# Kernel optimization log

Hardware: AMD Instinct MI355X
Metric: run time of the kernel (lower is better)

Reference implementation:

```python
import jax, jax.numpy as jnp
import numpy as np

N_NODES = 50000
N_EDGES = 1600000
IN_CH = 128
HIDDEN = 64
OUT_DIM = 64
N_GRAPHS = 64


def setup_inputs() -> dict:
    key = jax.random.key(0)
    ks = jax.random.split(key, 8)
    x = jax.random.normal(ks[0], (N_NODES, IN_CH), dtype=jnp.float32)
    W1 = jax.random.normal(ks[1], (IN_CH, HIDDEN), dtype=jnp.float32) * (1.0 / np.sqrt(IN_CH))
    b1 = jnp.zeros((HIDDEN,), dtype=jnp.float32)
    W2 = jax.random.normal(ks[2], (HIDDEN, HIDDEN), dtype=jnp.float32) * (1.0 / np.sqrt(HIDDEN))
    b2 = jnp.zeros((HIDDEN,), dtype=jnp.float32)
    Wp = jax.random.normal(ks[3], (HIDDEN, OUT_DIM), dtype=jnp.float32) * (1.0 / np.sqrt(HIDDEN))
    bp = jnp.zeros((OUT_DIM,), dtype=jnp.float32)
    edge_index = jax.random.randint(ks[4], (2, N_EDGES), 0, N_NODES, dtype=jnp.int32)
    batch = jnp.sort(jax.random.randint(ks[5], (N_NODES,), 0, N_GRAPHS, dtype=jnp.int32))
    return {"x": x, "W1": W1, "b1": b1, "W2": W2, "b2": b2,
            "Wp": Wp, "bp": bp, "edge_index": edge_index, "batch": batch}


def _gcn_norm(edge_index, num_nodes):
    # add self-loops, then symmetric normalization D^{-1/2} (A+I) D^{-1/2}
    loop = jnp.arange(num_nodes, dtype=edge_index.dtype)
    src = jnp.concatenate([edge_index[0], loop])
    dst = jnp.concatenate([edge_index[1], loop])
    deg = jax.ops.segment_sum(jnp.ones_like(dst, dtype=jnp.float32), dst,
                              num_segments=num_nodes)
    dinv = jnp.where(deg > 0, jax.lax.rsqrt(deg), 0.0)
    norm = dinv[src] * dinv[dst]  # [E+N]
    return src, dst, norm


def _gcn_conv(x, W, b, src, dst, norm, num_nodes):
    h = x @ W                                  # [N, F_out] transform first (F_out small)
    msg = h[src] * norm[:, None]               # gather + scale  [E+N, F_out]
    agg = jax.ops.segment_sum(msg, dst, num_segments=num_nodes)
    return agg + b


def reference(x, W1, b1, W2, b2, Wp, bp, edge_index, batch):
    n = x.shape[0]
    src, dst, norm = _gcn_norm(edge_index, n)
    h = jax.nn.relu(_gcn_conv(x, W1, b1, src, dst, norm, n))
    # dropout: eval mode (identity)
    h = jax.nn.relu(_gcn_conv(h, W2, b2, src, dst, norm, n))
    # global mean pool over graphs in batch
    gsum = jax.ops.segment_sum(h, batch, num_segments=N_GRAPHS)
    cnt = jax.ops.segment_sum(jnp.ones((n,), dtype=h.dtype), batch,
                              num_segments=N_GRAPHS)
    g = gsum / jnp.maximum(cnt, 1.0)[:, None]
    return g @ Wp + bp
```

## Files before the change

### kernel.cpp

```cpp
#include <hip/hip_runtime.h>

#define N_NODES  50000
#define N_EDGESC 1600000
#define N_GRAPHS 64
#define NBUCK    196
#define CHUNK    2048
#define NBLK     782

static __device__ __forceinline__ unsigned short f2bf(float f) {
  unsigned u = __float_as_uint(f);
  u += 0x7FFF + ((u >> 16) & 1);
  return (unsigned short)(u >> 16);
}
static __device__ __forceinline__ float bfLo(unsigned u) {
  return __uint_as_float(u << 16);
}
static __device__ __forceinline__ float bfHi(unsigned u) {
  return __uint_as_float(u & 0xFFFF0000u);
}

static __device__ __forceinline__ int lowerb(const int* a, int n, int v) {
  int lo = 0, hi = n;
  while (lo < hi) { int m = (lo + hi) >> 1; if (a[m] < v) lo = m + 1; else hi = m; }
  return lo;
}

__global__ __launch_bounds__(256) void k_hist(const int* __restrict__ dst,
                                              int* __restrict__ bcnt,
                                              float* __restrict__ gsum, int E) {
  __shared__ int hist[NBUCK];
  int t = threadIdx.x, blk = blockIdx.x;
  if (t < NBUCK) hist[t] = 0;
  if (blk == 0) {
    for (int i = t; i < N_GRAPHS * 64; i += 256) gsum[i] = 0.f;
  }
  __syncthreads();
  int e0 = blk * CHUNK;
#pragma unroll
  for (int i = 0; i < CHUNK; i += 256) {
    int e = e0 + i + t;
    if (e < E) atomicAdd(&hist[dst[e] >> 8], 1);
  }
  __syncthreads();
  if (t < NBUCK) bcnt[(size_t)t * NBLK + blk] = hist[t];
}

__global__ __launch_bounds__(256) void k_cscan(int* __restrict__ bcnt,
                                               int* __restrict__ btot) {
  __shared__ int sm[256];
  int b = blockIdx.x, t = threadIdx.x;
  int* p = bcnt + (size_t)b * NBLK;
  int carry = 0;
  for (int tile = 0; tile < (NBLK + 255) / 256; ++tile) {
    int idx = tile * 256 + t;
    int v = (idx < NBLK) ? p[idx] : 0;
    sm[t] = v;
    __syncthreads();
    for (int o = 1; o < 256; o <<= 1) {
      int add = (t >= o) ? sm[t - o] : 0;
      __syncthreads();
      sm[t] += add;
      __syncthreads();
    }
    int incl = sm[t];
    int total = sm[255];
    if (idx < NBLK) p[idx] = incl - v + carry;
    carry += total;
    __syncthreads();
  }
  if (t == 0) btot[b] = carry;
}

__global__ __launch_bounds__(256) void k_scatter(const int* __restrict__ src,
                                                 const int* __restrict__ dst,
                                                 const int* __restrict__ bcnt,
                                                 const int* __restrict__ btot,
                                                 unsigned* __restrict__ bbuf, int E) {
  __shared__ int base[NBUCK], cur[NBUCK], sm[256];
  int t = threadIdx.x, blk = blockIdx.x;
  int v = (t < NBUCK) ? btot[t] : 0;
  sm[t] = v;
  __syncthreads();
  for (int o = 1; o < 256; o <<= 1) {
    int add = (t >= o) ? sm[t - o] : 0;
    __syncthreads();
    sm[t] += add;
    __syncthreads();
  }
  if (t < NBUCK) {
    base[t] = (sm[t] - v) + bcnt[(size_t)t * NBLK + blk];
    cur[t] = 0;
  }
  __syncthreads();
  int e0 = blk * CHUNK;
#pragma unroll
  for (int i = 0; i < CHUNK; i += 256) {
    int e = e0 + i + t;
    if (e < E) {
      int d = dst[e], b = d >> 8;
      int pos = base[b] + atomicAdd(&cur[b], 1);
      bbuf[pos] = ((unsigned)(d & 255) << 24) | (unsigned)src[e];
    }
  }
}

__global__ __launch_bounds__(512) void k_bsort(const unsigned* __restrict__ bbuf,
                                               const int* __restrict__ btot,
                                               int* __restrict__ csr,
                                               int* __restrict__ row_off,
                                               float* __restrict__ dinv) {
  __shared__ int hist[256], off[256], cur[256], sm[256];
  int b = blockIdx.x, t = threadIdx.x;
  if (t < 256) {
    int v = (t < NBUCK) ? btot[t] : 0;
    sm[t] = v;
    hist[t] = 0; cur[t] = 0;
  }
  __syncthreads();
  for (int o = 1; o < 256; o <<= 1) {
    int add = 0;
    if (t < 256 && t >= o) add = sm[t - o];
    __syncthreads();
    if (t < 256) sm[t] += add;
    __syncthreads();
  }
  int gb = (b > 0) ? sm[b - 1] : 0;
  int cnt = btot[b];
  const unsigned* bp = bbuf + gb;
  for (int i = t; i < cnt; i += 512) atomicAdd(&hist[bp[i] >> 24], 1);
  __syncthreads();
  if (t < 256) off[t] = hist[t];
  __syncthreads();
  for (int o = 1; o < 256; o <<= 1) {
    int add = 0;
    if (t < 256 && t >= o) add = off[t - o];
    __syncthreads();
    if (t < 256) off[t] += add;
    __syncthreads();
  }
  if (t < 256) {
    int excl = off[t] - hist[t];
    off[t] = excl;
    int idx = (b << 8) + t;
    if (idx <= N_NODES) row_off[idx] = gb + excl;
    if (idx < N_NODES)  dinv[idx] = rsqrtf((float)(hist[t] + 1));
  }
  __syncthreads();
  for (int i = t; i < cnt; i += 512) {
    unsigned v = bp[i];
    int ld = v >> 24;
    int pos = atomicAdd(&cur[ld], 1);
    csr[gb + off[ld] + pos] = (int)(v & 0xFFFFFFu);
  }
}

template <int K>
__global__ __launch_bounds__(256) void k_gemm(const float* __restrict__ x,
                                              const float* __restrict__ W,
                                              const float* __restrict__ dinv,
                                              unsigned short* __restrict__ out, int N) {
  constexpr int KS = 64;
  constexpr int KP = KS + 4;
  __shared__ float xs[64 * KP];
  __shared__ float Wl[KS * 64];
  const int t = threadIdx.x;
  const int lane = t & 63;
  const int w = t >> 6;
  const int n0 = blockIdx.x * 64;

  float acc[16];
#pragma unroll
  for (int j = 0; j < 16; ++j) acc[j] = 0.f;

  for (int h = 0; h < K / KS; ++h) {
#pragma unroll
    for (int i = 0; i < KS * 16 / 256; ++i) {
      int li = i * 256 + t;
      float4 v = reinterpret_cast<const float4*>(W + h * KS * 64)[li];
      *reinterpret_cast<float4*>(Wl + li * 4) = v;
    }
#pragma unroll
    for (int i = 0; i < 64 * (KS / 4) / 256; ++i) {
      int li = i * 256 + t;
      int row = li / (KS / 4), c4 = li % (KS / 4);
      int node = n0 + row;
      float4 v = make_float4(0.f, 0.f, 0.f, 0.f);
      if (node < N) v = reinterpret_cast<const float4*>(x + (size_t)node * K + h * KS)[c4];
      *reinterpret_cast<float4*>(xs + row * KP + c4 * 4) = v;
    }
    __syncthreads();

    const float* xr = xs + lane * KP;
    const float* wq = Wl + w * 16;
#pragma unroll 4
    for (int kp = 0; kp < KS / 4; ++kp) {
      float4 xv = *reinterpret_cast<const float4*>(xr + kp * 4);
#pragma unroll
      for (int q = 0; q < 4; ++q) {
        int k = kp * 4 + q;
        float xq = (q == 0) ? xv.x : (q == 1) ? xv.y : (q == 2) ? xv.z : xv.w;
        const float* wk = wq + k * 64;
        float4 w0 = *reinterpret_cast<const float4*>(wk);
        float4 w1 = *reinterpret_cast<const float4*>(wk + 4);
        float4 w2 = *reinterpret_cast<const float4*>(wk + 8);
        float4 w3 = *reinterpret_cast<const float4*>(wk + 12);
        acc[ 0] = fmaf(xq, w0.x, acc[ 0]);
        acc[ 1] = fmaf(xq, w0.y, acc[ 1]);
        acc[ 2] = fmaf(xq, w0.z, acc[ 2]);
        acc[ 3] = fmaf(xq, w0.w, acc[ 3]);
        acc[ 4] = fmaf(xq, w1.x, acc[ 4]);
        acc[ 5] = fmaf(xq, w1.y, acc[ 5]);
        acc[ 6] = fmaf(xq, w1.z, acc[ 6]);
        acc[ 7] = fmaf(xq, w1.w, acc[ 7]);
        acc[ 8] = fmaf(xq, w2.x, acc[ 8]);
        acc[ 9] = fmaf(xq, w2.y, acc[ 9]);
        acc[10] = fmaf(xq, w2.z, acc[10]);
        acc[11] = fmaf(xq, w2.w, acc[11]);
        acc[12] = fmaf(xq, w3.x, acc[12]);
        acc[13] = fmaf(xq, w3.y, acc[13]);
        acc[14] = fmaf(xq, w3.z, acc[14]);
        acc[15] = fmaf(xq, w3.w, acc[15]);
      }
    }
    __syncthreads();
  }

  int node = n0 + lane;
  if (node < N) {
    float dv = dinv[node];
    unsigned pk[8];
#pragma unroll
    for (int j = 0; j < 8; ++j) {
      unsigned lo = f2bf(acc[2 * j] * dv);
      unsigned hi = f2bf(acc[2 * j + 1] * dv);
      pk[j] = lo | (hi << 16);
    }
    unsigned* op = reinterpret_cast<unsigned*>(out + (size_t)node * 64 + w * 16);
    *reinterpret_cast<uint4*>(op)     = make_uint4(pk[0], pk[1], pk[2], pk[3]);
    *reinterpret_cast<uint4*>(op + 4) = make_uint4(pk[4], pk[5], pk[6], pk[7]);
  }
}

__global__ __launch_bounds__(256) void k_gather(const unsigned short* __restrict__ hs,
                                                const int* __restrict__ row_off,
                                                const int* __restrict__ csr,
                                                const float* __restrict__ dinv,
                                                const float* __restrict__ bias,
                                                float* __restrict__ out, int N) {
  const int lane = threadIdx.x & 63;
  const int slot = lane >> 3;
  const int pos  = lane & 7;
  int n0 = (blockIdx.x * 4 + (threadIdx.x >> 6)) * 8;
  if (n0 >= N) return;
  const int node = n0 + slot;
  const uint4* hsq = reinterpret_cast<const uint4*>(hs);
  float4 bA = reinterpret_cast<const float4*>(bias)[pos * 2];
  float4 bB = reinterpret_cast<const float4*>(bias)[pos * 2 + 1];

  const int s0 = row_off[node];
  const int deg = row_off[node + 1] - s0;

  float a[8];
  {
    uint4 sv = hsq[(((unsigned)node) << 3) + pos];
    a[0] = bfLo(sv.x); a[1] = bfHi(sv.x); a[2] = bfLo(sv.y); a[3] = bfHi(sv.y);
    a[4] = bfLo(sv.z); a[5] = bfHi(sv.z); a[6] = bfLo(sv.w); a[7] = bfHi(sv.w);
  }

  for (int e = 0; __any(e < deg); e += 4) {
    int id[4];
    bool ok[4];
#pragma unroll
    for (int q = 0; q < 4; ++q) {
      int ei = e + q;
      ok[q] = ei < deg;
      id[q] = csr[s0 + max(min(ei, deg - 1), 0)];
    }
    uint4 v[4];
#pragma unroll
    for (int q = 0; q < 4; ++q)
      v[q] = hsq[(((unsigned)id[q]) << 3) + pos];
#pragma unroll
    for (int q = 0; q < 4; ++q) {
      if (ok[q]) {
        a[0] += bfLo(v[q].x); a[1] += bfHi(v[q].x);
        a[2] += bfLo(v[q].y); a[3] += bfHi(v[q].y);
        a[4] += bfLo(v[q].z); a[5] += bfHi(v[q].z);
        a[6] += bfLo(v[q].w); a[7] += bfHi(v[q].w);
      }
    }
  }

  float dv = dinv[node];
  float4 rA, rB;
  rA.x = fmaxf(fmaf(a[0], dv, bA.x), 0.f);
  rA.y = fmaxf(fmaf(a[1], dv, bA.y), 0.f);
  rA.z = fmaxf(fmaf(a[2], dv, bA.z), 0.f);
  rA.w = fmaxf(fmaf(a[3], dv, bA.w), 0.f);
  rB.x = fmaxf(fmaf(a[4], dv, bB.x), 0.f);
  rB.y = fmaxf(fmaf(a[5], dv, bB.y), 0.f);
  rB.z = fmaxf(fmaf(a[6], dv, bB.z), 0.f);
  rB.w = fmaxf(fmaf(a[7], dv, bB.w), 0.f);
  float4* op = reinterpret_cast<float4*>(out + (((size_t)node) << 6) + pos * 8);
  op[0] = rA;
  op[1] = rB;
}

__global__ __launch_bounds__(256) void k_pool1(const float* __restrict__ h,
                                               const int* __restrict__ batch,
                                               float* __restrict__ gsum, int N) {
  int c = threadIdx.x & 63;
  int w = threadIdx.x >> 6;
  int r0 = blockIdx.x * 64 + w * 16;
  if (r0 >= N) return;
  int r1 = min(r0 + 16, N);
  int gprev = batch[r0];
  float acc = 0.f;
  for (int r = r0; r < r1; ++r) {
    int g = batch[r];
    if (g != gprev) { atomicAdd(&gsum[gprev * 64 + c], acc); acc = 0.f; gprev = g; }
    acc += h[(size_t)r * 64 + c];
  }
  atomicAdd(&gsum[gprev * 64 + c], acc);
}

__global__ void k_final(const float* __restrict__ gsum, const int* __restrict__ batch,
                        const float* __restrict__ Wp, const float* __restrict__ bp,
                        float* __restrict__ out, int N) {
  __shared__ int lb[5];
  int t = threadIdx.x;
  int g0 = blockIdx.x * 4;
  if (t < 5) lb[t] = lowerb(batch, N, g0 + t);
  __syncthreads();
  int idx = blockIdx.x * 256 + t;
  int g = idx >> 6, o = idx & 63, gl = g & 3;
  float cinv = 1.0f / fmaxf((float)(lb[gl + 1] - lb[gl]), 1.0f);
  float acc = 0.f;
#pragma unroll
  for (int k = 0; k < 64; ++k) acc += gsum[g * 64 + k] * Wp[k * 64 + o];
  out[idx] = fmaf(acc, cinv, bp[o]);
}

extern "C" void kernel_launch(void* const* d_in, const int* in_sizes, int n_in,
                              void* d_out, int out_size, void* d_ws, size_t ws_size,
                              hipStream_t stream) {
  const float* x    = (const float*)d_in[0];
  const float* W1   = (const float*)d_in[1];
  const float* b1   = (const float*)d_in[2];
  const float* W2   = (const float*)d_in[3];
  const float* b2   = (const float*)d_in[4];
  const float* Wp   = (const float*)d_in[5];
  const float* bp   = (const float*)d_in[6];
  const int*   ei   = (const int*)d_in[7];
  const int*   batch= (const int*)d_in[8];
  float* out = (float*)d_out;

  const int N = N_NODES, E = N_EDGESC;
  const int* src  = ei;
  const int* dstp = ei + E;

  char* wsb = (char*)d_ws;
  size_t o = 0;
  auto alloc = [&](size_t bytes) -> void* {
    void* p = wsb + o;
    o = (o + bytes + 255) & ~(size_t)255;
    return p;
  };
  int*      bcnt   = (int*)alloc((size_t)NBUCK * NBLK * 4);
  int*      btot   = (int*)alloc(NBUCK * 4);
  unsigned* bbuf   = (unsigned*)alloc((size_t)E * 4);
  int*      row_off= (int*)alloc((size_t)(N + 1) * 4);
  int*      csr    = (int*)alloc((size_t)E * 4);
  float*    dinv   = (float*)alloc((size_t)N * 4);
  unsigned short* bufBF = (unsigned short*)alloc((size_t)N * 64 * 2);
  float*    bufF   = (float*)alloc((size_t)N * 64 * 4);
  float*    gsum   = (float*)alloc(64 * 64 * 4);

  int gN64 = (N + 63) / 64;
  int gG   = (N + 31) / 32;

  k_hist<<<NBLK, 256, 0, stream>>>(dstp, bcnt, gsum, E);
  k_cscan<<<NBUCK, 256, 0, stream>>>(bcnt, btot);
  k_scatter<<<NBLK, 256, 0, stream>>>(src, dstp, bcnt, btot, bbuf, E);
  k_bsort<<<NBUCK, 512, 0, stream>>>(bbuf, btot, csr, row_off, dinv);

  k_gemm<128><<<gN64, 256, 0, stream>>>(x, W1, dinv, bufBF, N);
  k_gather<<<gG, 256, 0, stream>>>(bufBF, row_off, csr, dinv, b1, bufF, N);
  k_gemm<64><<<gN64, 256, 0, stream>>>(bufF, W2, dinv, bufBF, N);
  k_gather<<<gG, 256, 0, stream>>>(bufBF, row_off, csr, dinv, b2, bufF, N);

  k_pool1<<<gN64, 256, 0, stream>>>(bufF, batch, gsum, N);
  k_final<<<16, 256, 0, stream>>>(gsum, batch, Wp, bp, out, N);
}
```

Before: 161.3 us.

## Sort nodes by degree within buckets to balance gather wavefront work

Inside the bucket-sort kernel, each 256-node bucket's nodes are bitonic-sorted by in-degree and a permutation array is written out. The gather kernels then process nodes in that order, so the 8 nodes sharing a wavefront have similar degrees and fewer lanes sit idle in the __any-driven edge loop. The cost is a shared-memory bitonic sort per bucket, an extra perm indirection, and scattered output writes and row_off reads.

```diff
diff --git a/kernel.cpp b/kernel.cpp
--- a/kernel.cpp
+++ b/kernel.cpp
@@ -6,6 +6,7 @@
 #define NBUCK    196
 #define CHUNK    2048
 #define NBLK     782
+#define NPERM    (NBUCK * 256)
 
 static __device__ __forceinline__ unsigned short f2bf(float f) {
   unsigned u = __float_as_uint(f);
@@ -108,8 +109,9 @@
                                                const int* __restrict__ btot,
                                                int* __restrict__ csr,
                                                int* __restrict__ row_off,
-                                               float* __restrict__ dinv) {
-  __shared__ int hist[256], off[256], cur[256], sm[256];
+                                               float* __restrict__ dinv,
+                                               int* __restrict__ perm) {
+  __shared__ int hist[256], off[256], cur[256], sm[256], skey[256];
   int b = blockIdx.x, t = threadIdx.x;
   if (t < 256) {
     int v = (t < NBUCK) ? btot[t] : 0;
@@ -144,6 +146,7 @@
     int idx = (b << 8) + t;
     if (idx <= N_NODES) row_off[idx] = gb + excl;
     if (idx < N_NODES)  dinv[idx] = rsqrtf((float)(hist[t] + 1));
+    skey[t] = (idx < N_NODES) ? ((hist[t] << 16) | t) : 0x7FFFFFFF;
   }
   __syncthreads();
   for (int i = t; i < cnt; i += 512) {
@@ -151,6 +154,24 @@
     int ld = v >> 24;
     int pos = atomicAdd(&cur[ld], 1);
     csr[gb + off[ld] + pos] = (int)(v & 0xFFFFFFu);
+  }
+  for (int k2 = 2; k2 <= 256; k2 <<= 1) {
+    for (int j = k2 >> 1; j > 0; j >>= 1) {
+      __syncthreads();
+      if (t < 256) {
+        int p = t ^ j;
+        if (p > t) {
+          int a = skey[t], c = skey[p];
+          bool up = ((t & k2) == 0);
+          if ((a > c) == up) { skey[t] = c; skey[p] = a; }
+        }
+      }
+    }
+  }
+  __syncthreads();
+  if (t < 256) {
+    int kv = skey[t];
+    perm[(b << 8) + t] = (kv == 0x7FFFFFFF) ? -1 : ((b << 8) + (kv & 0xFFFF));
   }
 }
 
@@ -246,23 +267,25 @@
                                                 const int* __restrict__ csr,
                                                 const float* __restrict__ dinv,
                                                 const float* __restrict__ bias,
-                                                float* __restrict__ out, int N) {
+                                                const int* __restrict__ perm,
+                                                float* __restrict__ out) {
   const int lane = threadIdx.x & 63;
   const int slot = lane >> 3;
   const int pos  = lane & 7;
-  int n0 = (blockIdx.x * 4 + (threadIdx.x >> 6)) * 8;
-  if (n0 >= N) return;
-  const int node = n0 + slot;
+  int p0 = (blockIdx.x * 4 + (threadIdx.x >> 6)) * 8;
+  const int node = perm[p0 + slot];
+  const bool live = node >= 0;
+  const int nid = live ? node : 0;
   const uint4* hsq = reinterpret_cast<const uint4*>(hs);
   float4 bA = reinterpret_cast<const float4*>(bias)[pos * 2];
   float4 bB = reinterpret_cast<const float4*>(bias)[pos * 2 + 1];
 
-  const int s0 = row_off[node];
-  const int deg = row_off[node + 1] - s0;
+  int s0 = 0, deg = 0;
+  if (live) { s0 = row_off[nid]; deg = row_off[nid + 1] - s0; }
 
   float a[8];
   {
-    uint4 sv = hsq[(((unsigned)node) << 3) + pos];
+    uint4 sv = hsq[(((unsigned)nid) << 3) + pos];
     a[0] = bfLo(sv.x); a[1] = bfHi(sv.x); a[2] = bfLo(sv.y); a[3] = bfHi(sv.y);
     a[4] = bfLo(sv.z); a[5] = bfHi(sv.z); a[6] = bfLo(sv.w); a[7] = bfHi(sv.w);
   }
@@ -291,19 +314,21 @@
     }
   }
 
-  float dv = dinv[node];
-  float4 rA, rB;
-  rA.x = fmaxf(fmaf(a[0], dv, bA.x), 0.f);
-  rA.y = fmaxf(fmaf(a[1], dv, bA.y), 0.f);
-  rA.z = fmaxf(fmaf(a[2], dv, bA.z), 0.f);
-  rA.w = fmaxf(fmaf(a[3], dv, bA.w), 0.f);
-  rB.x = fmaxf(fmaf(a[4], dv, bB.x), 0.f);
-  rB.y = fmaxf(fmaf(a[5], dv, bB.y), 0.f);
-  rB.z = fmaxf(fmaf(a[6], dv, bB.z), 0.f);
-  rB.w = fmaxf(fmaf(a[7], dv, bB.w), 0.f);
-  float4* op = reinterpret_cast<float4*>(out + (((size_t)node) << 6) + pos * 8);
-  op[0] = rA;
-  op[1] = rB;
+  if (live) {
+    float dv = dinv[nid];
+    float4 rA, rB;
+    rA.x = fmaxf(fmaf(a[0], dv, bA.x), 0.f);
+    rA.y = fmaxf(fmaf(a[1], dv, bA.y), 0.f);
+    rA.z = fmaxf(fmaf(a[2], dv, bA.z), 0.f);
+    rA.w = fmaxf(fmaf(a[3], dv, bA.w), 0.f);
+    rB.x = fmaxf(fmaf(a[4], dv, bB.x), 0.f);
+    rB.y = fmaxf(fmaf(a[5], dv, bB.y), 0.f);
+    rB.z = fmaxf(fmaf(a[6], dv, bB.z), 0.f);
+    rB.w = fmaxf(fmaf(a[7], dv, bB.w), 0.f);
+    float4* op = reinterpret_cast<float4*>(out + (((size_t)nid) << 6) + pos * 8);
+    op[0] = rA;
+    op[1] = rB;
+  }
 }
 
 __global__ __launch_bounds__(256) void k_pool1(const float* __restrict__ h,
@@ -372,22 +397,23 @@
   int*      row_off= (int*)alloc((size_t)(N + 1) * 4);
   int*      csr    = (int*)alloc((size_t)E * 4);
   float*    dinv   = (float*)alloc((size_t)N * 4);
+  int*      perm   = (int*)alloc((size_t)NPERM * 4);
   unsigned short* bufBF = (unsigned short*)alloc((size_t)N * 64 * 2);
   float*    bufF   = (float*)alloc((size_t)N * 64 * 4);
   float*    gsum   = (float*)alloc(64 * 64 * 4);
 
   int gN64 = (N + 63) / 64;
-  int gG   = (N + 31) / 32;
+  int gG   = NPERM / 32;
 
   k_hist<<<NBLK, 256, 0, stream>>>(dstp, bcnt, gsum, E);
   k_cscan<<<NBUCK, 256, 0, stream>>>(bcnt, btot);
   k_scatter<<<NBLK, 256, 0, stream>>>(src, dstp, bcnt, btot, bbuf, E);
-  k_bsort<<<NBUCK, 512, 0, stream>>>(bbuf, btot, csr, row_off, dinv);
+  k_bsort<<<NBUCK, 512, 0, stream>>>(bbuf, btot, csr, row_off, dinv, perm);
 
   k_gemm<128><<<gN64, 256, 0, stream>>>(x, W1, dinv, bufBF, N);
-  k_gather<<<gG, 256, 0, stream>>>(bufBF, row_off, csr, dinv, b1, bufF, N);
+  k_gather<<<gG, 256, 0, stream>>>(bufBF, row_off, csr, dinv, b1, perm, bufF);
   k_gemm<64><<<gN64, 256, 0, stream>>>(bufF, W2, dinv, bufBF, N);
-  k_gather<<<gG, 256, 0, stream>>>(bufBF, row_off, csr, dinv, b2, bufF, N);
+  k_gather<<<gG, 256, 0, stream>>>(bufBF, row_off, csr, dinv, b2, perm, bufF);
 
   k_pool1<<<gN64, 256, 0, stream>>>(bufF, batch, gsum, N);
   k_final<<<16, 256, 0, stream>>>(gsum, batch, Wp, bp, out, N);
```

Measured after the change: 172.6 us. 1.07x slower.
